# Performance work log

Measured on AMD Instinct MI355X. Metric: run time of the kernel, lower is better.

## Reference

```python
import jax, jax.numpy as jnp
import numpy as np

B, T, C = 2, 2048, 1024
H, D = 16, 64            # num_heads, head_dim
R_W, R_A, R_G = 64, 64, 160  # lora low-rank dims per __init__ formulas
EPS = D * 1e-5           # GroupNorm eps = head_dim * norm_eps


def setup_inputs() -> dict:
    key = jax.random.key(0)
    ks = jax.random.split(key, 28)
    n = lambda k, s, sc=1.0: jax.random.normal(k, s, jnp.float32) * sc
    u = lambda k, s: jax.random.uniform(k, s, jnp.float32)
    return {
        'hidden_states': n(ks[0], (B, T, C)),
        # token-shift mixing coefficients
        'x_r': u(ks[1], (1, 1, C)), 'x_w': u(ks[2], (1, 1, C)),
        'x_k': u(ks[3], (1, 1, C)), 'x_v': u(ks[4], (1, 1, C)),
        'x_a': u(ks[5], (1, 1, C)), 'x_g': u(ks[6], (1, 1, C)),
        'k_k': 0.71 + n(ks[7], (C,), 0.05),
        'k_a': 1.02 + n(ks[8], (C,), 0.05),
        'r_k': -0.04 + n(ks[9], (H, D), 0.02),
        # projections (torch Linear convention: (out, in))
        'Wr': n(ks[10], (C, C), 0.02), 'Wk': n(ks[11], (C, C), 0.02),
        'Wv': n(ks[12], (C, C), 0.02), 'Wo': n(ks[13], (C, C), 0.02),
        # decay LoRA (tanh activation, bias)
        'w_lora_A': n(ks[14], (R_W, C), 0.02),
        'w_lora_B': n(ks[15], (C, R_W), 0.02),
        'w_lora_bias': n(ks[16], (C,), 0.5),
        # in-context-learning-rate LoRA (no activation, bias)
        'a_lora_A': n(ks[17], (R_A, C), 0.02),
        'a_lora_B': n(ks[18], (C, R_A), 0.02),
        'a_lora_bias': n(ks[19], (C,), 0.3),
        # gate LoRA (sigmoid activation, no bias)
        'g_lora_A': n(ks[20], (R_G, C), 0.02),
        'g_lora_B': n(ks[21], (C, R_G), 0.02),
        # GroupNorm affine
        'gn_weight': jnp.ones((C,), jnp.float32) * 0.8,
        'gn_bias': n(ks[22], (C,), 0.01),
        # PoST decay bias parameterization
        'w0_base': jnp.asarray(-6.0, jnp.float32),
        'w0_delta': n(ks[23], (C - 1,), 0.1) - 5.0,
    }


def _lin(x, W):  # torch nn.Linear: y = x @ W.T
    return jnp.einsum('btc,oc->bto', x, W)


def reference(hidden_states, x_r, x_w, x_k, x_v, x_a, x_g, k_k, k_a, r_k,
              Wr, Wk, Wv, Wo,
              w_lora_A, w_lora_B, w_lora_bias,
              a_lora_A, a_lora_B, a_lora_bias,
              g_lora_A, g_lora_B,
              gn_weight, gn_bias, w0_base, w0_delta):
    x = hidden_states
    # time_shift = ZeroPad2d((0,0,1,-1)): shifted[t] = x[t-1], shifted[0] = 0
    shifted = jnp.pad(x, ((0, 0), (1, 0), (0, 0)))[:, :-1]
    delta = shifted - x
    xr = x + delta * x_r
    xw = x + delta * x_w
    xk = x + delta * x_k
    xv = x + delta * x_v
    xa = x + delta * x_a
    xg = x + delta * x_g

    r = _lin(xr, Wr)
    k = _lin(xk, Wk)
    v = _lin(xv, Wv)

    # PoST map: w0_k = w0_base + cumsum(softplus(delta)) -> strictly increasing
    gaps = jax.nn.softplus(w0_delta)
    w0 = w0_base + jnp.concatenate([jnp.zeros((1,), gaps.dtype), jnp.cumsum(gaps)])
    w_lr = jnp.einsum('btr,cr->btc', jnp.tanh(_lin(xw, w_lora_A)), w_lora_B) + w_lora_bias
    w = -jax.nn.softplus(-(w0 + w_lr)) - 0.5      # log-log decay, in (-inf, -0.5]
    decay = jnp.exp(-jnp.exp(w))                  # per-channel decay in (0, 1)

    a = jax.nn.sigmoid(
        jnp.einsum('btr,cr->btc', _lin(xa, a_lora_A), a_lora_B) + a_lora_bias)
    g = jnp.einsum('btr,cr->btc', jax.nn.sigmoid(_lin(xg, g_lora_A)), g_lora_B)

    kk = (k * k_k).reshape(B, T, H, D)
    kk = kk / jnp.maximum(jnp.linalg.norm(kk, axis=-1, keepdims=True), 1e-12)
    k = k * (1.0 + (a - 1.0) * k_a)

    rh = r.reshape(B, T, H, D)
    kh = k.reshape(B, T, H, D)
    vh = v.reshape(B, T, H, D)
    ah = a.reshape(B, T, H, D)
    wh = decay.reshape(B, T, H, D)
    a_in = -kk          # removal direction
    b_in = kk * ah      # replacement strength

    # RWKV-7 recurrence: S_t = S_{t-1} diag(w_t) + (S_{t-1} a_t) b_t^T + v_t k_t^T
    # state S: (B, H, D_v, D_k); output o_t = S_t r_t
    def step(S, ins):
        q_t, w_t, k_t, v_t, a_t, b_t = ins  # each (B, H, D)
        sa = jnp.einsum('bhik,bhk->bhi', S, a_t)
        S = (S * w_t[:, :, None, :]
             + sa[..., None] * b_t[:, :, None, :]
             + v_t[..., None] * k_t[:, :, None, :])
        o_t = jnp.einsum('bhik,bhk->bhi', S, q_t)
        return S, o_t

    tr = lambda z: jnp.transpose(z, (1, 0, 2, 3))  # (B,T,H,D) -> (T,B,H,D)
    S0 = jnp.zeros((B, H, D, D), x.dtype)
    _, o = jax.lax.scan(step, S0, (tr(rh), tr(wh), tr(kh), tr(vh), tr(a_in), tr(b_in)))
    o = jnp.transpose(o, (1, 0, 2, 3))  # (B, T, H, D)

    # GroupNorm with num_groups = H over flattened (B*T, C)
    mu = o.mean(-1, keepdims=True)
    var = o.var(-1, keepdims=True)
    on = ((o - mu) / jnp.sqrt(var + EPS)).reshape(B, T, C) * gn_weight + gn_bias

    # per-head bonus term
    bonus = ((rh * kh * r_k).sum(-1, keepdims=True) * vh).reshape(B, T, C)

    out = _lin((on + bonus) * g, Wo)
    return out
```

## Files before the change

### kernel.cpp

```cpp
#include <hip/hip_runtime.h>
#include <hip/hip_bf16.h>
#include <math.h>

typedef float f32x4 __attribute__((ext_vector_type(4)));
typedef short s16x8 __attribute__((ext_vector_type(8)));
typedef short s16x4 __attribute__((ext_vector_type(4)));

#define TSEQ 2048

__device__ __forceinline__ unsigned short f2bf(float f){
  unsigned int u = __builtin_bit_cast(unsigned int, f);
  u += 0x7FFFu + ((u >> 16) & 1u);
  return (unsigned short)(u >> 16);
}
__device__ __forceinline__ float sigf(float x){ return 1.0f / (1.0f + __expf(-x)); }
__device__ __forceinline__ float wredsum(float x){
  #pragma unroll
  for (int off = 32; off > 0; off >>= 1) x += __shfl_xor(x, off);
  return x;
}

template<int CTRL>
__device__ __forceinline__ float dpp_add(float x){
  int v = __builtin_amdgcn_update_dpp(0, __builtin_bit_cast(int, x), CTRL, 0xF, 0xF, true);
  return x + __builtin_bit_cast(float, v);
}
__device__ __forceinline__ float red16(float x){
  x = dpp_add<0xB1>(x);
  x = dpp_add<0x4E>(x);
  x = dpp_add<0x124>(x);
  x = dpp_add<0x128>(x);
  return x;
}

__device__ __forceinline__ void g2l16(const unsigned short* gp, void* lp){
  __builtin_amdgcn_global_load_lds(
    (const __attribute__((address_space(1))) unsigned int*)gp,
    (__attribute__((address_space(3))) unsigned int*)lp, 16, 0, 0);
}
__device__ __forceinline__ void g2l16f(const float* gp, void* lp){
  __builtin_amdgcn_global_load_lds(
    (const __attribute__((address_space(1))) unsigned int*)gp,
    (__attribute__((address_space(3))) unsigned int*)lp, 16, 0, 0);
}

__global__ void w0_scan_k(const float* __restrict__ w0b, const float* __restrict__ w0d,
                          float* __restrict__ w0){
  __shared__ float buf[1024];
  int i = threadIdx.x;
  float v = 0.f;
  if (i > 0){
    float d = w0d[i-1];
    v = (d > 20.f) ? d : log1pf(__expf(d));
  }
  buf[i] = v;
  __syncthreads();
  for (int off = 1; off < 1024; off <<= 1){
    float t = (i >= off) ? buf[i - off] : 0.f;
    __syncthreads();
    buf[i] += t;
    __syncthreads();
  }
  w0[i] = w0b[0] + buf[i];
}

struct WCvtArgs { const float* src[10]; };
__constant__ const int WCSUM[11] = {0, 1048576, 2097152, 3145728, 4194304,
                                    4259840, 4325376, 4390912, 4456448, 4620288, 4784128};
#define WTOT 4784128

__global__ __launch_bounds__(256) void wcvt_k(WCvtArgs args, unsigned short* __restrict__ dst){
  const int e0 = (blockIdx.x * 256 + threadIdx.x) * 4;
  #pragma unroll
  for (int i = 0; i < 10; i++){
    if (e0 < WCSUM[i+1]){
      const f32x4 q = *(const f32x4*)(args.src[i] + (e0 - WCSUM[i]));
      s16x4 o; o[0]=(short)f2bf(q.x); o[1]=(short)f2bf(q.y); o[2]=(short)f2bf(q.z); o[3]=(short)f2bf(q.w);
      *(s16x4*)(dst + e0) = o;
      return;
    }
  }
}

__global__ __launch_bounds__(256) void prep_k(
    const float* __restrict__ x,
    const float* __restrict__ cr, const float* __restrict__ cw, const float* __restrict__ ck,
    const float* __restrict__ cv, const float* __restrict__ ca, const float* __restrict__ cg,
    unsigned short* __restrict__ xr, unsigned short* __restrict__ xw, unsigned short* __restrict__ xk,
    unsigned short* __restrict__ xv, unsigned short* __restrict__ xa, unsigned short* __restrict__ xg)
{
  const int m = blockIdx.x;
  const int c = threadIdx.x * 4;
  const size_t ix = (size_t)m * 1024 + c;
  const f32x4 q = *(const f32x4*)(x + ix);
  f32x4 s = {0.f,0.f,0.f,0.f};
  if ((m & (TSEQ - 1)) != 0) s = *(const f32x4*)(x + ix - 1024);
  const f32x4 d = s - q;
  #define DO_MIX(coef, out) { \
    const f32x4 mc = *(const f32x4*)(coef + c); \
    s16x4 o; \
    o[0]=(short)f2bf(fmaf(d.x, mc.x, q.x)); o[1]=(short)f2bf(fmaf(d.y, mc.y, q.y)); \
    o[2]=(short)f2bf(fmaf(d.z, mc.z, q.z)); o[3]=(short)f2bf(fmaf(d.w, mc.w, q.w)); \
    *(s16x4*)(out + ix) = o; }
  DO_MIX(cr, xr); DO_MIX(cw, xw); DO_MIX(ck, xk);
  DO_MIX(cv, xv); DO_MIX(ca, xa); DO_MIX(cg, xg);
  #undef DO_MIX
}

#define EPI_F32 0
#define EPI_BF16 1
#define EPI_TANH_BF16 2
#define EPI_SIG_BF16 3
#define EPI_PK_F32 4
#define EPI_PK_SIG 5
#define EPI_PK_DECAY 6

template<int EPI, int ARR>
__global__ __launch_bounds__(256) void gemm_k(
    const unsigned short* __restrict__ ABF,
    const unsigned short* __restrict__ BBF,
    void* __restrict__ Cout,
    const float* __restrict__ bias, const float* __restrict__ w0,
    int M, int N, int K)
{
  __shared__ unsigned short As[2][64][32];
  __shared__ unsigned short Bs[2][128][32];
  const int tid  = threadIdx.x;
  const int m0   = blockIdx.y * 64;
  const int n0   = blockIdx.x * 128;
  const int srow = tid >> 2;
  const int scol = (tid & 3) << 3;
  const int wofs = (tid >> 6) << 10;
  const int lane = tid & 63;
  const int wv   = tid >> 6;
  const int wr   = (wv >> 1) << 5;
  const int wc   = (wv & 1) << 6;
  const int lr   = lane & 15;
  const int lg   = lane >> 4;

#define STAGE(BUF, KOFF) { \
    const unsigned short* a0 = ABF + (size_t)(m0 + srow) * K + (KOFF) + scol; \
    const unsigned short* b0 = BBF + (size_t)(n0 + srow) * K + (KOFF) + scol; \
    g2l16(a0,                 (char*)&As[BUF][0][0] + wofs); \
    g2l16(b0,                 (char*)&Bs[BUF][0][0] + wofs); \
    g2l16(b0 + (size_t)64*K,  (char*)&Bs[BUF][0][0] + 4096 + wofs); }

  f32x4 acc[2][4];
  #pragma unroll
  for (int i = 0; i < 2; i++)
    #pragma unroll
    for (int j = 0; j < 4; j++) acc[i][j] = f32x4{0.f, 0.f, 0.f, 0.f};

  STAGE(0, 0)
  __syncthreads();

  int buf = 0;
  for (int k0 = 0; k0 < K; k0 += 32){
    if (k0 + 32 < K){ STAGE(buf ^ 1, k0 + 32) }
    s16x8 af[2], bfr[4];
    #pragma unroll
    for (int i = 0; i < 2; i++) af[i]  = *(const s16x8*)&As[buf][wr + i*16 + lr][lg*8];
    #pragma unroll
    for (int j = 0; j < 4; j++) bfr[j] = *(const s16x8*)&Bs[buf][wc + j*16 + lr][lg*8];
    #pragma unroll
    for (int i = 0; i < 2; i++)
      #pragma unroll
      for (int j = 0; j < 4; j++)
        acc[i][j] = __builtin_amdgcn_mfma_f32_16x16x32_bf16(af[i], bfr[j], acc[i][j], 0, 0, 0);
    __syncthreads();
    buf ^= 1;
  }
#undef STAGE

  #pragma unroll
  for (int i = 0; i < 2; i++){
    const int mb = m0 + wr + i*16 + lg*4;
    #pragma unroll
    for (int j = 0; j < 4; j++){
      const int n = n0 + wc + j*16 + lr;
      if (n < N){
        #pragma unroll
        for (int q = 0; q < 4; q++){
          const int m = mb + q;
          const float val = acc[i][j][q];
          if constexpr (EPI == EPI_PK_F32 || EPI == EPI_PK_SIG || EPI == EPI_PK_DECAY){
            const int b2 = m >> 11, t2 = m & 2047, h2 = n >> 6, ch = n & 63;
            const size_t pix = (size_t)(b2*16 + h2) * (TSEQ*384) + (size_t)t2*384 + ARR*64 + ch;
            if constexpr (EPI == EPI_PK_F32) ((float*)Cout)[pix] = val;
            else if constexpr (EPI == EPI_PK_SIG) ((float*)Cout)[pix] = sigf(val + bias[n]);
            else {
              float z = val + bias[n] + w0[n];
              ((float*)Cout)[pix] = expf(-0.60653065971263342f * sigf(z));
            }
          } else {
            const size_t oix = (size_t)m * N + n;
            if constexpr (EPI == EPI_F32)            ((float*)Cout)[oix] = val;
            else if constexpr (EPI == EPI_BF16)      ((unsigned short*)Cout)[oix] = f2bf(val);
            else if constexpr (EPI == EPI_TANH_BF16) ((unsigned short*)Cout)[oix] = f2bf(tanhf(val));
            else if constexpr (EPI == EPI_SIG_BF16)  ((unsigned short*)Cout)[oix] = f2bf(sigf(val));
          }
        }
      }
    }
  }
}

__global__ __launch_bounds__(256) void kkprep2_k(
    float* __restrict__ pk, const float* __restrict__ kkc, const float* __restrict__ kac)
{
  const int flat = blockIdx.x * 4 + (threadIdx.x >> 6);
  const int lane = threadIdx.x & 63;
  const int bh = flat >> 11, t = flat & 2047;
  const size_t pb = (size_t)bh * (TSEQ*384) + (size_t)t * 384;
  const int c = (bh & 15) * 64 + lane;
  const float kraw = pk[pb + 128 + lane];
  const float araw = pk[pb + 192 + lane];
  const float tt = kraw * kkc[c];
  const float ss = wredsum(tt * tt);
  const float kkv = tt / fmaxf(sqrtf(ss), 1e-12f);
  pk[pb + 128 + lane] = kraw * (1.f + (araw - 1.f) * kac[c]);
  pk[pb + 192 + lane] = kkv * araw;
  pk[pb + 256 + lane] = -kkv;
}

__global__ __launch_bounds__(64) void scan_k(
    const float* __restrict__ pk, float* __restrict__ o)
{
  const int lane = threadIdx.x;
  const int L = lane & 15, g = lane >> 4;
  const int f = blockIdx.x;
  const int grp = (f >> 3) & 15;
  const int bh  = ((f >> 7) << 3) | (f & 7);
  const int b_  = bh >> 4, h_ = bh & 15;
  const size_t pkb = (size_t)bh * (TSEQ * 384);
  const int vq = 4 * L;
  const int vrow = grp * 4 + g;

  __shared__ float lds[8][1536];
  int mload = 0;

#define G2LG(SLOT) { \
    const int mc = (mload < TSEQ/4) ? mload : (TSEQ/4 - 1); \
    const float* src = pk + pkb + (size_t)mc * 1536 + lane * 4; \
    g2l16f(src +    0, &lds[SLOT][0]);    \
    g2l16f(src +  256, &lds[SLOT][256]);  \
    g2l16f(src +  512, &lds[SLOT][512]);  \
    g2l16f(src +  768, &lds[SLOT][768]);  \
    g2l16f(src + 1024, &lds[SLOT][1024]); \
    g2l16f(src + 1280, &lds[SLOT][1280]); \
    mload++; }

  f32x4 Rg[4], Wg[4], Kg[4], Bg[4], Ag[4]; float Vg[4];

#define PREF1(SLOT, I, SET) { \
    const float* pb_ = &lds[SLOT][(I)*384]; \
    Rg[SET] = *(const f32x4*)(pb_ + vq); \
    Wg[SET] = *(const f32x4*)(pb_ + 64 + vq); \
    Kg[SET] = *(const f32x4*)(pb_ + 128 + vq); \
    Bg[SET] = *(const f32x4*)(pb_ + 192 + vq); \
    Ag[SET] = *(const f32x4*)(pb_ + 256 + vq); \
    Vg[SET] = pb_[320 + vrow]; }
#define PREF2(SLOT, HALF, S0, S1) PREF1(SLOT,(HALF)*2,S0) PREF1(SLOT,(HALF)*2+1,S1)

  f32x4 S = {0.f, 0.f, 0.f, 0.f};
  float oreg = 0.f;

#define STEP(I, SIDX) { \
    const float p = fmaf(S.y, Ag[I].y, S.x * Ag[I].x) + fmaf(S.w, Ag[I].w, S.z * Ag[I].z); \
    const float sa = red16(p); \
    const float cv = Vg[I]; \
    S.x = fmaf(S.x, Wg[I].x, fmaf(sa, Bg[I].x, cv * Kg[I].x)); \
    S.y = fmaf(S.y, Wg[I].y, fmaf(sa, Bg[I].y, cv * Kg[I].y)); \
    S.z = fmaf(S.z, Wg[I].z, fmaf(sa, Bg[I].z, cv * Kg[I].z)); \
    S.w = fmaf(S.w, Wg[I].w, fmaf(sa, Bg[I].w, cv * Kg[I].w)); \
    const float q = fmaf(S.y, Rg[I].y, S.x * Rg[I].x) + fmaf(S.w, Rg[I].w, S.z * Rg[I].z); \
    const float oo = red16(q); \
    oreg = (L == (SIDX)) ? oo : oreg; }

#define VMW(N) asm volatile("s_waitcnt vmcnt(" #N ")" ::: "memory");

#define HSEQA(J, SX) \
    PREF2(J, 1, 2, 3) \
    STEP(0, (SX)+0) STEP(1, (SX)+1)

#define HSEQB(J, SX) \
    VMW(36) \
    PREF2(((J)+1)&7, 0, 0, 1) \
    STEP(2, (SX)+2) STEP(3, (SX)+3) \
    G2LG(J)

  G2LG(0) G2LG(1) G2LG(2) G2LG(3) G2LG(4) G2LG(5) G2LG(6) G2LG(7)
  VMW(42)
  PREF2(0, 0, 0, 1)

  const size_t ob = (size_t)b_ * (TSEQ*1024) + h_*64;
  for (int ot = 0; ot < TSEQ/32; ++ot){
    HSEQA(0,0)  HSEQB(0,0)
    HSEQA(1,4)  HSEQB(1,4)
    HSEQA(2,8)  HSEQB(2,8)
    HSEQA(3,12) HSEQB(3,12)
    o[ob + (size_t)(32*ot + L) * 1024 + vrow] = oreg;
    HSEQA(4,0)  HSEQB(4,0)
    HSEQA(5,4)  HSEQB(5,4)
    HSEQA(6,8)  HSEQB(6,8)
    HSEQA(7,12) HSEQB(7,12)
    o[ob + (size_t)(32*ot + 16 + L) * 1024 + vrow] = oreg;
  }

#undef G2LG
#undef PREF1
#undef PREF2
#undef STEP
#undef VMW
#undef HSEQA
#undef HSEQB
}

__global__ __launch_bounds__(256) void gnout_k(
    const float* __restrict__ pk, const float* __restrict__ o, const float* __restrict__ g_,
    const float* __restrict__ rk, const float* __restrict__ gnw, const float* __restrict__ gnb,
    unsigned short* __restrict__ y)
{
  const int flat = blockIdx.x * 4 + (threadIdx.x >> 6);
  const int lane = threadIdx.x & 63;
  const int bh = flat >> 11, t = flat & 2047;
  const int b_ = bh >> 4, h_ = bh & 15;
  const size_t pb = (size_t)bh * (TSEQ*384) + (size_t)t * 384;
  const int c = h_*64 + lane;
  const size_t fi = (size_t)(b_*2048 + t) * 1024 + c;
  const float rv = pk[pb + lane];
  const float kv = pk[pb + 128 + lane];
  const float vv = pk[pb + 320 + lane];
  const float ov = o[fi];
  const float mu  = wredsum(ov) * 0.015625f;
  const float d   = ov - mu;
  const float var = wredsum(d * d) * 0.015625f;
  const float on  = d * rsqrtf(var + 6.4e-4f) * gnw[c] + gnb[c];
  const float s   = wredsum(rv * kv * rk[c]);
  const float yv  = (on + s * vv) * g_[fi];
  y[fi] = f2bf(yv);
}

extern "C" void kernel_launch(void* const* d_in, const int* in_sizes, int n_in,
                              void* d_out, int out_size, void* d_ws, size_t ws_size,
                              hipStream_t stream)
{
  const float* x    = (const float*)d_in[0];
  const float* x_r  = (const float*)d_in[1];
  const float* x_w  = (const float*)d_in[2];
  const float* x_k  = (const float*)d_in[3];
  const float* x_v  = (const float*)d_in[4];
  const float* x_a  = (const float*)d_in[5];
  const float* x_g  = (const float*)d_in[6];
  const float* k_k  = (const float*)d_in[7];
  const float* k_a  = (const float*)d_in[8];
  const float* r_k  = (const float*)d_in[9];
  const float* Wr   = (const float*)d_in[10];
  const float* Wk   = (const float*)d_in[11];
  const float* Wv   = (const float*)d_in[12];
  const float* Wo   = (const float*)d_in[13];
  const float* wA   = (const float*)d_in[14];
  const float* wB   = (const float*)d_in[15];
  const float* wbias= (const float*)d_in[16];
  const float* aA   = (const float*)d_in[17];
  const float* aB   = (const float*)d_in[18];
  const float* abias= (const float*)d_in[19];
  const float* gA   = (const float*)d_in[20];
  const float* gB   = (const float*)d_in[21];
  const float* gnw  = (const float*)d_in[22];
  const float* gnb  = (const float*)d_in[23];
  const float* w0b  = (const float*)d_in[24];
  const float* w0d  = (const float*)d_in[25];

  char* ws = (char*)d_ws;
  const size_t MB = 1024ull * 1024ull;
  const size_t KB = 1024ull;

  float*          pk_  = (float*)(ws + 0);
  unsigned short* xw_  = (unsigned short*)(ws + 0*MB);
  unsigned short* xa_  = (unsigned short*)(ws + 8*MB);
  unsigned short* xg_  = (unsigned short*)(ws + 16*MB);
  float*          g_   = (float*)(ws + 96*MB);
  unsigned short* xr_  = (unsigned short*)(ws + 96*MB);
  unsigned short* xk_  = (unsigned short*)(ws + 104*MB);
  unsigned short* y_   = (unsigned short*)(ws + 112*MB);
  unsigned short* xv_  = (unsigned short*)(ws + 112*MB);
  unsigned short* wbf_ = (unsigned short*)(ws + 120*MB);
  unsigned short* wl1_ = (unsigned short*)(ws + 130*MB);
  unsigned short* al1_ = (unsigned short*)(ws + 130*MB + 512*KB);
  unsigned short* gl1_ = (unsigned short*)(ws + 131*MB);
  float*          w0_  = (float*)(ws + 132*MB + 512*KB);
  float*          o_   = (float*)(ws + 133*MB);

  const unsigned short* bWr = wbf_ + 0;
  const unsigned short* bWk = wbf_ + 1048576;
  const unsigned short* bWv = wbf_ + 2097152;
  const unsigned short* bWo = wbf_ + 3145728;
  const unsigned short* bwA = wbf_ + 4194304;
  const unsigned short* bwB = wbf_ + 4259840;
  const unsigned short* baA = wbf_ + 4325376;
  const unsigned short* baB = wbf_ + 4390912;
  const unsigned short* bgA = wbf_ + 4456448;
  const unsigned short* bgB = wbf_ + 4620288;

  const dim3 blk(256);
  const dim3 gBig(8, 64), gN64(1, 64), gN160(2, 64);

  w0_scan_k<<<dim3(1), dim3(1024), 0, stream>>>(w0b, w0d, w0_);

  WCvtArgs wargs;
  wargs.src[0]=Wr; wargs.src[1]=Wk; wargs.src[2]=Wv; wargs.src[3]=Wo;
  wargs.src[4]=wA; wargs.src[5]=wB; wargs.src[6]=aA; wargs.src[7]=aB;
  wargs.src[8]=gA; wargs.src[9]=gB;
  wcvt_k<<<dim3(WTOT/4/256), blk, 0, stream>>>(wargs, wbf_);

  prep_k<<<dim3(4096), blk, 0, stream>>>(x, x_r, x_w, x_k, x_v, x_a, x_g,
                                         xr_, xw_, xk_, xv_, xa_, xg_);

  gemm_k<EPI_TANH_BF16,0><<<gN64, blk, 0, stream>>>(xw_, bwA, wl1_, nullptr, nullptr, 4096, 64, 1024);
  gemm_k<EPI_BF16,0><<<gN64, blk, 0, stream>>>(xa_, baA, al1_, nullptr, nullptr, 4096, 64, 1024);
  gemm_k<EPI_SIG_BF16,0><<<gN160, blk, 0, stream>>>(xg_, bgA, gl1_, nullptr, nullptr, 4096, 160, 1024);

  gemm_k<EPI_PK_F32,0><<<gBig, blk, 0, stream>>>(xr_, bWr, pk_, nullptr, nullptr, 4096, 1024, 1024);
  gemm_k<EPI_PK_F32,2><<<gBig, blk, 0, stream>>>(xk_, bWk, pk_, nullptr, nullptr, 4096, 1024, 1024);
  gemm_k<EPI_PK_F32,5><<<gBig, blk, 0, stream>>>(xv_, bWv, pk_, nullptr, nullptr, 4096, 1024, 1024);

  gemm_k<EPI_PK_DECAY,1><<<gBig, blk, 0, stream>>>(wl1_, bwB, pk_, wbias, w0_, 4096, 1024, 64);
  gemm_k<EPI_PK_SIG,3><<<gBig, blk, 0, stream>>>(al1_, baB, pk_, abias, nullptr, 4096, 1024, 64);

  gemm_k<EPI_F32,0><<<gBig, blk, 0, stream>>>(gl1_, bgB, g_, nullptr, nullptr, 4096, 1024, 160);

  kkprep2_k<<<dim3(16384), blk, 0, stream>>>(pk_, k_k, k_a);

  scan_k<<<dim3(512), dim3(64), 0, stream>>>(pk_, o_);

  gnout_k<<<dim3(16384), blk, 0, stream>>>(pk_, o_, g_, r_k, gnw, gnb, y_);

  gemm_k<EPI_F32,0><<<gBig, blk, 0, stream>>>(y_, bWo, (float*)d_out, nullptr, nullptr, 4096, 1024, 1024);
}
```

Before: 448.6 us.

## Split scan rows across four waves with one state element per lane

```diff
diff --git a/kernel.cpp b/kernel.cpp
--- a/kernel.cpp
+++ b/kernel.cpp
@@ -20,17 +20,22 @@
   return x;
 }
 
-template<int CTRL>
+template<int CTRL, int RM>
 __device__ __forceinline__ float dpp_add(float x){
-  int v = __builtin_amdgcn_update_dpp(0, __builtin_bit_cast(int, x), CTRL, 0xF, 0xF, true);
+  int v = __builtin_amdgcn_update_dpp(0, __builtin_bit_cast(int, x), CTRL, RM, 0xF, true);
   return x + __builtin_bit_cast(float, v);
 }
-__device__ __forceinline__ float red16(float x){
-  x = dpp_add<0xB1>(x);
-  x = dpp_add<0x4E>(x);
-  x = dpp_add<0x124>(x);
-  x = dpp_add<0x128>(x);
+__device__ __forceinline__ float red64(float x){
+  x = dpp_add<0xB1,  0xF>(x);
+  x = dpp_add<0x4E,  0xF>(x);
+  x = dpp_add<0x124, 0xF>(x);
+  x = dpp_add<0x128, 0xF>(x);
+  x = dpp_add<0x142, 0xA>(x);
+  x = dpp_add<0x143, 0xC>(x);
   return x;
+}
+__device__ __forceinline__ float rl63(float x){
+  return __builtin_bit_cast(float, __builtin_amdgcn_readlane(__builtin_bit_cast(int, x), 63));
 }
 
 __device__ __forceinline__ void g2l16(const unsigned short* gp, void* lp){
@@ -223,59 +228,60 @@
   pk[pb + 256 + lane] = -kkv;
 }
 
-__global__ __launch_bounds__(64) void scan_k(
+__global__ __launch_bounds__(256) void scan_k(
     const float* __restrict__ pk, float* __restrict__ o)
 {
-  const int lane = threadIdx.x;
-  const int L = lane & 15, g = lane >> 4;
-  const int f = blockIdx.x;
-  const int grp = (f >> 3) & 15;
-  const int bh  = ((f >> 7) << 3) | (f & 7);
-  const int b_  = bh >> 4, h_ = bh & 15;
+  const int tid  = threadIdx.x;
+  const int lane = tid & 63;
+  const int wv   = tid >> 6;
+  const int f    = blockIdx.x;
+  const int grp  = (f >> 3) & 15;
+  const int bh   = ((f >> 7) << 3) | (f & 7);
+  const int b_   = bh >> 4, h_ = bh & 15;
   const size_t pkb = (size_t)bh * (TSEQ * 384);
-  const int vq = 4 * L;
-  const int vrow = grp * 4 + g;
+  const int row  = grp * 4 + wv;
 
   __shared__ float lds[8][1536];
   int mload = 0;
 
 #define G2LG(SLOT) { \
-    const int mc = (mload < TSEQ/4) ? mload : (TSEQ/4 - 1); \
-    const float* src = pk + pkb + (size_t)mc * 1536 + lane * 4; \
-    g2l16f(src +    0, &lds[SLOT][0]);    \
-    g2l16f(src +  256, &lds[SLOT][256]);  \
-    g2l16f(src +  512, &lds[SLOT][512]);  \
-    g2l16f(src +  768, &lds[SLOT][768]);  \
-    g2l16f(src + 1024, &lds[SLOT][1024]); \
-    g2l16f(src + 1280, &lds[SLOT][1280]); \
+    if (wv == 0){ \
+      const int mc = (mload < TSEQ/4) ? mload : (TSEQ/4 - 1); \
+      const float* src = pk + pkb + (size_t)mc * 1536 + lane * 4; \
+      g2l16f(src +    0, &lds[SLOT][0]);    \
+      g2l16f(src +  256, &lds[SLOT][256]);  \
+      g2l16f(src +  512, &lds[SLOT][512]);  \
+      g2l16f(src +  768, &lds[SLOT][768]);  \
+      g2l16f(src + 1024, &lds[SLOT][1024]); \
+      g2l16f(src + 1280, &lds[SLOT][1280]); \
+    } \
     mload++; }
 
-  f32x4 Rg[4], Wg[4], Kg[4], Bg[4], Ag[4]; float Vg[4];
+  f32x4 dummy; (void)dummy;
+  float Rg[4], Wg[4], Kg[4], Bg[4], Ag[4], Vg[4];
 
 #define PREF1(SLOT, I, SET) { \
     const float* pb_ = &lds[SLOT][(I)*384]; \
-    Rg[SET] = *(const f32x4*)(pb_ + vq); \
-    Wg[SET] = *(const f32x4*)(pb_ + 64 + vq); \
-    Kg[SET] = *(const f32x4*)(pb_ + 128 + vq); \
-    Bg[SET] = *(const f32x4*)(pb_ + 192 + vq); \
-    Ag[SET] = *(const f32x4*)(pb_ + 256 + vq); \
-    Vg[SET] = pb_[320 + vrow]; }
+    Rg[SET] = pb_[lane]; \
+    Wg[SET] = pb_[64 + lane]; \
+    Kg[SET] = pb_[128 + lane]; \
+    Bg[SET] = pb_[192 + lane]; \
+    Ag[SET] = pb_[256 + lane]; \
+    Vg[SET] = pb_[320 + row]; }
 #define PREF2(SLOT, HALF, S0, S1) PREF1(SLOT,(HALF)*2,S0) PREF1(SLOT,(HALF)*2+1,S1)
 
-  f32x4 S = {0.f, 0.f, 0.f, 0.f};
+  float S = 0.f;
   float oreg = 0.f;
 
 #define STEP(I, SIDX) { \
-    const float p = fmaf(S.y, Ag[I].y, S.x * Ag[I].x) + fmaf(S.w, Ag[I].w, S.z * Ag[I].z); \
-    const float sa = red16(p); \
-    const float cv = Vg[I]; \
-    S.x = fmaf(S.x, Wg[I].x, fmaf(sa, Bg[I].x, cv * Kg[I].x)); \
-    S.y = fmaf(S.y, Wg[I].y, fmaf(sa, Bg[I].y, cv * Kg[I].y)); \
-    S.z = fmaf(S.z, Wg[I].z, fmaf(sa, Bg[I].z, cv * Kg[I].z)); \
-    S.w = fmaf(S.w, Wg[I].w, fmaf(sa, Bg[I].w, cv * Kg[I].w)); \
-    const float q = fmaf(S.y, Rg[I].y, S.x * Rg[I].x) + fmaf(S.w, Rg[I].w, S.z * Rg[I].z); \
-    const float oo = red16(q); \
-    oreg = (L == (SIDX)) ? oo : oreg; }
+    float p = S * Ag[I]; \
+    p = red64(p); \
+    const float sa = rl63(p); \
+    S = fmaf(S, Wg[I], fmaf(sa, Bg[I], Vg[I] * Kg[I])); \
+    float q = S * Rg[I]; \
+    q = red64(q); \
+    const float sq = rl63(q); \
+    oreg = (lane == (SIDX)) ? sq : oreg; }
 
 #define VMW(N) asm volatile("s_waitcnt vmcnt(" #N ")" ::: "memory");
 
@@ -285,26 +291,35 @@
 
 #define HSEQB(J, SX) \
     VMW(36) \
+    __builtin_amdgcn_s_barrier(); \
     PREF2(((J)+1)&7, 0, 0, 1) \
     STEP(2, (SX)+2) STEP(3, (SX)+3) \
     G2LG(J)
 
   G2LG(0) G2LG(1) G2LG(2) G2LG(3) G2LG(4) G2LG(5) G2LG(6) G2LG(7)
   VMW(42)
+  __builtin_amdgcn_s_barrier();
   PREF2(0, 0, 0, 1)
 
-  const size_t ob = (size_t)b_ * (TSEQ*1024) + h_*64;
-  for (int ot = 0; ot < TSEQ/32; ++ot){
-    HSEQA(0,0)  HSEQB(0,0)
-    HSEQA(1,4)  HSEQB(1,4)
-    HSEQA(2,8)  HSEQB(2,8)
-    HSEQA(3,12) HSEQB(3,12)
-    o[ob + (size_t)(32*ot + L) * 1024 + vrow] = oreg;
-    HSEQA(4,0)  HSEQB(4,0)
-    HSEQA(5,4)  HSEQB(5,4)
-    HSEQA(6,8)  HSEQB(6,8)
-    HSEQA(7,12) HSEQB(7,12)
-    o[ob + (size_t)(32*ot + 16 + L) * 1024 + vrow] = oreg;
+  const size_t ob = (size_t)b_ * (TSEQ*1024) + h_*64 + row;
+  for (int ow = 0; ow < TSEQ/64; ++ow){
+    HSEQA(0,0)   HSEQB(0,0)
+    HSEQA(1,4)   HSEQB(1,4)
+    HSEQA(2,8)   HSEQB(2,8)
+    HSEQA(3,12)  HSEQB(3,12)
+    HSEQA(4,16)  HSEQB(4,16)
+    HSEQA(5,20)  HSEQB(5,20)
+    HSEQA(6,24)  HSEQB(6,24)
+    HSEQA(7,28)  HSEQB(7,28)
+    HSEQA(0,32)  HSEQB(0,32)
+    HSEQA(1,36)  HSEQB(1,36)
+    HSEQA(2,40)  HSEQB(2,40)
+    HSEQA(3,44)  HSEQB(3,44)
+    HSEQA(4,48)  HSEQB(4,48)
+    HSEQA(5,52)  HSEQB(5,52)
+    HSEQA(6,56)  HSEQB(6,56)
+    HSEQA(7,60)  HSEQB(7,60)
+    o[ob + (size_t)(64*ow + lane) * 1024] = oreg;
   }
 
 #undef G2LG
@@ -432,7 +447,7 @@
 
   kkprep2_k<<<dim3(16384), blk, 0, stream>>>(pk_, k_k, k_a);
 
-  scan_k<<<dim3(512), dim3(64), 0, stream>>>(pk_, o_);
+  scan_k<<<dim3(512), blk, 0, stream>>>(pk_, o_);
 
   gnout_k<<<dim3(16384), blk, 0, stream>>>(pk_, o_, g_, r_k, gnw, gnb, y_);
 
```

New measurement: 549.1 us. 22.4% more time.
